# Optimization experiments

Hardware: AMD Instinct MI355X
Metric: run time of the kernel (lower is better)

The kernel has to match this reference:

```python
import jax, jax.numpy as jnp
import numpy as np
import math

N_HEADS = 16
D_KV = 64
D_MODEL = 1024
NUM_BUCKETS = 32
MAX_DISTANCE = 128


def _relative_position_bucket(rel_pos):
    # encoder (is_decoder=False): bidirectional buckets
    num_buckets = NUM_BUCKETS // 2  # 16
    rel_buckets = (rel_pos > 0).astype(jnp.int32) * num_buckets
    rel_pos = jnp.abs(rel_pos)
    max_exact = num_buckets // 2  # 8
    is_small = rel_pos < max_exact
    rel_pos_large = max_exact + (
        jnp.log(rel_pos.astype(jnp.float32) / max_exact)
        / math.log(MAX_DISTANCE / max_exact)
        * (num_buckets - max_exact)
    ).astype(jnp.int32)
    rel_pos_large = jnp.minimum(rel_pos_large, num_buckets - 1)
    return rel_buckets + jnp.where(is_small, rel_pos, rel_pos_large)


def setup_inputs() -> dict:
    key = jax.random.key(0)
    ks = jax.random.split(key, 6)
    s = 1.0 / math.sqrt(D_MODEL)
    return {
        "hidden_states": jax.random.normal(ks[0], (2, 2048, D_MODEL), jnp.float32),
        "Wq": jax.random.normal(ks[1], (D_MODEL, N_HEADS * D_KV), jnp.float32) * s,
        "Wk": jax.random.normal(ks[2], (D_MODEL, N_HEADS * D_KV), jnp.float32) * s,
        "Wv": jax.random.normal(ks[3], (D_MODEL, N_HEADS * D_KV), jnp.float32) * s,
        "Wo": jax.random.normal(ks[4], (N_HEADS * D_KV, D_MODEL), jnp.float32) * s,
        "rel_bias": jax.random.normal(ks[5], (NUM_BUCKETS, N_HEADS), jnp.float32),
    }


def reference(hidden_states, Wq, Wk, Wv, Wo, rel_bias):
    b, seq, _ = hidden_states.shape
    q = (hidden_states @ Wq).reshape(b, seq, N_HEADS, D_KV)
    k = (hidden_states @ Wk).reshape(b, seq, N_HEADS, D_KV)
    v = (hidden_states @ Wv).reshape(b, seq, N_HEADS, D_KV)

    # relative position bias: [1, n_heads, q_len, k_len]
    ctx = jnp.arange(seq, dtype=jnp.int32)[:, None]
    mem = jnp.arange(seq, dtype=jnp.int32)[None, :]
    buckets = _relative_position_bucket(mem - ctx)  # [q, k]
    pos_bias = rel_bias[buckets]                    # [q, k, h]
    pos_bias = jnp.transpose(pos_bias, (2, 0, 1))[None]  # [1, h, q, k]

    # NOTE: T5-style attention has no 1/sqrt(d) scaling
    attn = jnp.einsum('binc,bjnc->bnij', q, k) + pos_bias
    attn = jax.nn.softmax(attn.astype(jnp.float32), axis=-1).astype(attn.dtype)
    o = jnp.einsum('bnij,bjnc->binc', attn, v).reshape(b, seq, N_HEADS * D_KV)
    return o @ Wo
```

## Files before the change

### kernel.cpp

```cpp
#include <hip/hip_runtime.h>
#include <hip/hip_bf16.h>
#include <math.h>

#define DM   1024
#define HD   1024
#define NH   16
#define DK   64
#define SEQ  2048
#define BATCH 2

#define LOG2E 1.4426950408889634f

typedef __attribute__((ext_vector_type(8))) short bf16x8;
typedef __attribute__((ext_vector_type(4))) float f32x4;

static __device__ __forceinline__ short f2b(float f) {
  union { float f; unsigned u; } v; v.f = f;
  unsigned r = (v.u + 0x7fffu + ((v.u >> 16) & 1u)) >> 16;
  return (short)r;
}

static __device__ __forceinline__ void gload_lds16(const void* g, void* l) {
  __builtin_amdgcn_global_load_lds(
      (const __attribute__((address_space(1))) void*)g,
      (__attribute__((address_space(3))) void*)l, 16, 0, 0);
}


__global__ __launch_bounds__(256) void k_cvt_h(const float* __restrict__ in,
                                               short* __restrict__ out) {
  int i = (blockIdx.x * 256 + threadIdx.x) * 8;
  float4 a = *reinterpret_cast<const float4*>(in + i);
  float4 b = *reinterpret_cast<const float4*>(in + i + 4);
  bf16x8 o;
  o[0] = f2b(a.x); o[1] = f2b(a.y); o[2] = f2b(a.z); o[3] = f2b(a.w);
  o[4] = f2b(b.x); o[5] = f2b(b.y); o[6] = f2b(b.z); o[7] = f2b(b.w);
  *reinterpret_cast<bf16x8*>(out + i) = o;
}

__global__ __launch_bounds__(256) void k_wtrans(const float* __restrict__ Wq,
                                                const float* __restrict__ Wk,
                                                const float* __restrict__ Wv,
                                                const float* __restrict__ Wo,
                                                short* __restrict__ Wts) {
  const float* src = (blockIdx.z == 0) ? Wq : (blockIdx.z == 1) ? Wk
                   : (blockIdx.z == 2) ? Wv : Wo;
  const float scl = (blockIdx.z == 0) ? LOG2E : 1.0f;
  short* dst = Wts + (size_t)blockIdx.z * DM * HD;
  __shared__ float t[32][33];
  int tx = threadIdx.x & 31, ty = threadIdx.x >> 5;
  int k0 = blockIdx.y * 32, n0 = blockIdx.x * 32;
#pragma unroll
  for (int i = 0; i < 4; ++i)
    t[ty + i * 8][tx] = src[(size_t)(k0 + ty + i * 8) * 1024 + n0 + tx];
  __syncthreads();
#pragma unroll
  for (int i = 0; i < 4; ++i)
    dst[(size_t)(n0 + ty + i * 8) * 1024 + k0 + tx] = f2b(t[tx][ty + i * 8] * scl);
}

__global__ __launch_bounds__(256) void k_bias(const float* __restrict__ rel_bias,
                                              float* __restrict__ btab) {
  int idx = blockIdx.x * 256 + threadIdx.x;
  int h = idx >> 12, pos = idx & 4095;
  int delta = pos - 2047;
  int rb = (delta > 0) ? 16 : 0;
  int ar = (delta < 0) ? -delta : delta;
  int bb;
  if (ar < 8) bb = ar;
  else {
    bb = 8 + (int)(logf((float)ar * 0.125f) * (8.0f / 2.7725887222397811f));
    if (bb > 15) bb = 15;
  }
  btab[idx] = rel_bias[(rb + bb) * NH + h] * LOG2E;
}

__global__ __launch_bounds__(256) void k_vtrans(const short* __restrict__ Vb,
                                                short* __restrict__ Vt) {
  int bh = blockIdx.y, b = bh >> 4, h = bh & 15;
  int st = blockIdx.x * 64;
  __shared__ short t[64][72];
  int tx = threadIdx.x & 15, ty = threadIdx.x >> 4;
#pragma unroll
  for (int i = 0; i < 4; ++i) {
    int row = ty + i * 16;
    *reinterpret_cast<short4*>(&t[row][tx * 4]) =
        *reinterpret_cast<const short4*>(
            &Vb[(size_t)(b * SEQ + st + row) * HD + h * 64 + tx * 4]);
  }
  __syncthreads();
  const int chunk = tx >> 3, bb = tx & 7;
  const int p = ((bb & 3) << 1) | (bb >> 2);
  const int kvpos = st + chunk * 32 + p * 4;
#pragma unroll
  for (int i = 0; i < 4; ++i) {
    int dk = ty + i * 16;
    short4 v = make_short4(t[tx * 4 + 0][dk], t[tx * 4 + 1][dk],
                           t[tx * 4 + 2][dk], t[tx * 4 + 3][dk]);
    *reinterpret_cast<short4*>(
        &Vt[(size_t)bh * DK * SEQ + (size_t)dk * SEQ + kvpos]) = v;
  }
}

template <int OUTF32>
__global__ __launch_bounds__(256) void k_gemm_bt(const short* __restrict__ A,
                                                 const short* __restrict__ Bt,
                                                 void* __restrict__ Cv,
                                                 size_t btz, size_t cz) {
  __shared__ __align__(16) short As[128 * 32];
  __shared__ __align__(16) short Bs[128 * 32];
  const int tid = threadIdx.x, w = tid >> 6, lane = tid & 63;
  const int wr = w >> 1, wc = w & 1, lg = lane >> 4, l15 = lane & 15;
  const int rowBase = blockIdx.y * 128, colBase = blockIdx.x * 128;
  const short* B = Bt + (size_t)blockIdx.z * btz;

  f32x4 acc[4][4];
#pragma unroll
  for (int m = 0; m < 4; ++m)
#pragma unroll
    for (int n = 0; n < 4; ++n) acc[m][n] = (f32x4){0.f, 0.f, 0.f, 0.f};

  const int c1 = w * 64 + lane, c2 = c1 + 256;
  const short* Ap1 = A + (size_t)(rowBase + (c1 >> 2)) * 1024 + (c1 & 3) * 8;
  const short* Ap2 = A + (size_t)(rowBase + (c2 >> 2)) * 1024 + (c2 & 3) * 8;
  const short* Bp1 = B + (size_t)(colBase + (c1 >> 2)) * 1024 + (c1 & 3) * 8;
  const short* Bp2 = B + (size_t)(colBase + (c2 >> 2)) * 1024 + (c2 & 3) * 8;
  char* AsB = (char*)As;
  char* BsB = (char*)Bs;

  for (int k0 = 0; k0 < 1024; k0 += 32) {
    __syncthreads();
    gload_lds16(Ap1 + k0, AsB + w * 1024);
    gload_lds16(Ap2 + k0, AsB + 4096 + w * 1024);
    gload_lds16(Bp1 + k0, BsB + w * 1024);
    gload_lds16(Bp2 + k0, BsB + 4096 + w * 1024);
    asm volatile("s_waitcnt vmcnt(0)" ::: "memory");
    __syncthreads();
    bf16x8 af[4], bfr[4];
#pragma unroll
    for (int m = 0; m < 4; ++m)
      af[m] = *reinterpret_cast<const bf16x8*>(
          &As[(wr * 64 + m * 16 + l15) * 32 + lg * 8]);
#pragma unroll
    for (int n = 0; n < 4; ++n)
      bfr[n] = *reinterpret_cast<const bf16x8*>(
          &Bs[(wc * 64 + n * 16 + l15) * 32 + lg * 8]);
#pragma unroll
    for (int m = 0; m < 4; ++m)
#pragma unroll
      for (int n = 0; n < 4; ++n)
        acc[m][n] =
            __builtin_amdgcn_mfma_f32_16x16x32_bf16(af[m], bfr[n], acc[m][n], 0, 0, 0);
  }

#pragma unroll
  for (int m = 0; m < 4; ++m)
#pragma unroll
    for (int n = 0; n < 4; ++n) {
      int col = colBase + wc * 64 + n * 16 + l15;
#pragma unroll
      for (int r = 0; r < 4; ++r) {
        int row = rowBase + wr * 64 + m * 16 + lg * 4 + r;
        if (OUTF32)
          ((float*)Cv)[(size_t)row * 1024 + col] = acc[m][n][r];
        else
          ((short*)Cv + (size_t)blockIdx.z * cz)[(size_t)row * 1024 + col] =
              f2b(acc[m][n][r]);
      }
    }
}

static __device__ __forceinline__ void stage_tile(const char* gbase, size_t grs,
                                                  char* lbase, int w, int lane) {
  const int r0 = w * 16 + (lane >> 3);
  const int cb = (lane & 7) * 16;
  const int sw = (r0 & 7) << 4;
  gload_lds16(gbase + (size_t)r0 * grs + (cb ^ sw), lbase + w * 2048);
  gload_lds16(gbase + (size_t)(r0 + 8) * grs + (cb ^ sw), lbase + w * 2048 + 1024);
}

__global__ __launch_bounds__(256, 4) void k_attn(const short* __restrict__ Qb,
                                                 const short* __restrict__ Kb,
                                                 const short* __restrict__ Vt,
                                                 const float* __restrict__ biasTab,
                                                 short* __restrict__ Ob) {
  const int j = blockIdx.x;
  const int orig = (j & 7) * 128 + (j >> 3);
  const int qt = orig & 31, bh = orig >> 5;
  const int b = bh >> 4, h = bh & 15;
  const int w = threadIdx.x >> 6, lane = threadIdx.x & 63;
  const int lg = lane >> 4, l15 = lane & 15;
  const int qbase = qt * 64 + w * 16;

  __shared__ __align__(16) char Ks[2][8192];
  __shared__ __align__(16) char Vs[2][8192];
  const int swz = (l15 & 7) << 4;

  const short* Qrow = Qb + (size_t)(b * SEQ + qbase + l15) * HD + h * 64 + lg * 8;
  bf16x8 q0 = *reinterpret_cast<const bf16x8*>(Qrow);
  bf16x8 q1 = *reinterpret_cast<const bf16x8*>(Qrow + 32);

  const char* Kg = (const char*)(Kb + (size_t)(b * SEQ) * HD + h * 64);
  const char* Vg = (const char*)(Vt + (size_t)bh * DK * SEQ);
  const float* btab = biasTab + h * 4096 + 2047;
  const float bias_hi = btab[1024];
  const float bias_lo = btab[-1024];

  f32x4 o[4];
#pragma unroll
  for (int c = 0; c < 4; ++c) o[c] = (f32x4){0.f, 0.f, 0.f, 0.f};
  float m_r = -INFINITY, l_r = 0.f;

  const f32x4 z4 = (f32x4){0.f, 0.f, 0.f, 0.f};

  stage_tile(Kg, 2048, Ks[0], w, lane);
  stage_tile(Vg, 4096, Vs[0], w, lane);
  asm volatile("s_waitcnt vmcnt(0)" ::: "memory");
  __syncthreads();
  int cur = 0;

  for (int kt = 0; kt < 32; ++kt) {
    const int kvb = kt * 64;
    const int dkv = kvb - qbase;
    if (kt < 31) {
      stage_tile(Kg + (size_t)(kvb + 64) * 2048, 2048, Ks[cur ^ 1], w, lane);
      stage_tile(Vg + (size_t)(kvb + 64) * 2, 4096, Vs[cur ^ 1], w, lane);
    }
    const char* KsC = Ks[cur];
    f32x4 s[4];
#pragma unroll
    for (int c = 0; c < 4; ++c) {
      const char* kr = KsC + (c * 16 + l15) * 128;
      bf16x8 kf0 = *reinterpret_cast<const bf16x8*>(kr + ((lg * 16) ^ swz));
      bf16x8 kf1 = *reinterpret_cast<const bf16x8*>(kr + ((64 + lg * 16) ^ swz));
      s[c] = __builtin_amdgcn_mfma_f32_16x16x32_bf16(kf0, q0, z4, 0, 0, 0);
      s[c] = __builtin_amdgcn_mfma_f32_16x16x32_bf16(kf1, q1, s[c], 0, 0, 0);
    }
    if (dkv >= 112) {
#pragma unroll
      for (int c = 0; c < 4; ++c)
#pragma unroll
        for (int r = 0; r < 4; ++r) s[c][r] += bias_hi;
    } else if (dkv <= -160) {
#pragma unroll
      for (int c = 0; c < 4; ++c)
#pragma unroll
        for (int r = 0; r < 4; ++r) s[c][r] += bias_lo;
    } else {
#pragma unroll
      for (int c = 0; c < 4; ++c)
#pragma unroll
        for (int r = 0; r < 4; ++r)
          s[c][r] += btab[dkv + c * 16 + lg * 4 + r - l15];
    }
    float t0 = fmaxf(fmaxf(s[0][0], s[0][1]), fmaxf(s[0][2], s[0][3]));
    float t1 = fmaxf(fmaxf(s[1][0], s[1][1]), fmaxf(s[1][2], s[1][3]));
    float t2 = fmaxf(fmaxf(s[2][0], s[2][1]), fmaxf(s[2][2], s[2][3]));
    float t3 = fmaxf(fmaxf(s[3][0], s[3][1]), fmaxf(s[3][2], s[3][3]));
    float mx = fmaxf(fmaxf(t0, t1), fmaxf(t2, t3));
    mx = fmaxf(mx, __shfl_xor(mx, 16, 64));
    mx = fmaxf(mx, __shfl_xor(mx, 32, 64));
    if (!__all(mx <= m_r + 8.0f)) {
      float mn = fmaxf(m_r, mx);
      float sc = __builtin_exp2f(m_r - mn);
      m_r = mn;
      l_r *= sc;
#pragma unroll
      for (int c = 0; c < 4; ++c)
#pragma unroll
        for (int r = 0; r < 4; ++r) o[c][r] *= sc;
    }
#pragma unroll
    for (int c = 0; c < 4; ++c)
#pragma unroll
      for (int r = 0; r < 4; ++r) s[c][r] = __builtin_exp2f(s[c][r] - m_r);
    float r0 = (s[0][0] + s[0][1]) + (s[0][2] + s[0][3]);
    float r1 = (s[1][0] + s[1][1]) + (s[1][2] + s[1][3]);
    float r2 = (s[2][0] + s[2][1]) + (s[2][2] + s[2][3]);
    float r3 = (s[3][0] + s[3][1]) + (s[3][2] + s[3][3]);
    float rs = (r0 + r1) + (r2 + r3);
    rs += __shfl_xor(rs, 16, 64);
    rs += __shfl_xor(rs, 32, 64);
    l_r += rs;
    bf16x8 pb0, pb1;
#pragma unroll
    for (int r = 0; r < 4; ++r) {
      pb0[r]     = f2b(s[0][r]);
      pb0[4 + r] = f2b(s[1][r]);
      pb1[r]     = f2b(s[2][r]);
      pb1[4 + r] = f2b(s[3][r]);
    }
    const char* VsC = Vs[cur];
#pragma unroll
    for (int d = 0; d < 4; ++d) {
      const char* vr = VsC + (d * 16 + l15) * 128;
      bf16x8 v0 = *reinterpret_cast<const bf16x8*>(vr + ((lg * 16) ^ swz));
      bf16x8 v1 = *reinterpret_cast<const bf16x8*>(vr + ((64 + lg * 16) ^ swz));
      o[d] = __builtin_amdgcn_mfma_f32_16x16x32_bf16(v0, pb0, o[d], 0, 0, 0);
      o[d] = __builtin_amdgcn_mfma_f32_16x16x32_bf16(v1, pb1, o[d], 0, 0, 0);
    }
    asm volatile("s_waitcnt vmcnt(0)" ::: "memory");
    __syncthreads();
    cur ^= 1;
  }
  float inv = 1.0f / l_r;
  const size_t orow = (size_t)(b * SEQ + qbase + l15) * HD + h * 64;
#pragma unroll
  for (int d = 0; d < 4; ++d) {
    short4 pk;
    pk.x = f2b(o[d][0] * inv); pk.y = f2b(o[d][1] * inv);
    pk.z = f2b(o[d][2] * inv); pk.w = f2b(o[d][3] * inv);
    *reinterpret_cast<short4*>(&Ob[orow + d * 16 + lg * 4]) = pk;
  }
}

extern "C" void kernel_launch(void* const* d_in, const int* in_sizes, int n_in,
                              void* d_out, int out_size, void* d_ws, size_t ws_size,
                              hipStream_t stream) {
  const float* H    = (const float*)d_in[0];
  const float* Wq   = (const float*)d_in[1];
  const float* Wk   = (const float*)d_in[2];
  const float* Wv   = (const float*)d_in[3];
  const float* Wo   = (const float*)d_in[4];
  const float* relb = (const float*)d_in[5];

  char* ws = (char*)d_ws;
  short* Hb   = (short*)(ws);
  short* Wts  = (short*)(ws + ((size_t)8 << 20));
  short* Qb   = (short*)(ws + ((size_t)16 << 20));
  short* Kb   = (short*)(ws + ((size_t)24 << 20));
  short* Vb   = (short*)(ws + ((size_t)32 << 20));
  short* Vt   = (short*)(ws + ((size_t)40 << 20));
  short* Ob   = (short*)(ws + ((size_t)48 << 20));
  float* btab = (float*)(ws + ((size_t)56 << 20));

  k_cvt_h<<<2048, 256, 0, stream>>>(H, Hb);
  k_wtrans<<<dim3(32, 32, 4), 256, 0, stream>>>(Wq, Wk, Wv, Wo, Wts);
  k_bias<<<256, 256, 0, stream>>>(relb, btab);

  k_gemm_bt<0><<<dim3(8, 32, 3), 256, 0, stream>>>(
      Hb, Wts, Qb, (size_t)1024 * 1024, (size_t)4096 * 1024);

  k_vtrans<<<dim3(32, 32), 256, 0, stream>>>(Vb, Vt);
  k_attn<<<1024, 256, 0, stream>>>(Qb, Kb, Vt, btab, Ob);

  k_gemm_bt<1><<<dim3(8, 32, 1), 256, 0, stream>>>(
      Ob, Wts + (size_t)3 * 1024 * 1024, d_out, 0, 0);
}
```

Before: 234.2 us.

## Use packed bf16 convert, fold uniform bias into max, add MFMA priority hints

Replaces the software round-to-nearest bf16 conversion with the hardware v_cvt_pk_bf16_f32 instruction in the attention inner loop and the epilogue. For tiles where the relative-position bias is uniform, the bias is no longer added to all 16 scores; it is added once to the row max and subtracted from the exp2 offset instead. The max reduction is rebalanced into three-input fmax chains, and s_setprio is raised around the MFMA sections so waves issuing matrix ops get scheduling priority. The aim is fewer VALU instructions per tile in the softmax path. The hardware convert may round slightly differently from the software routine.

```diff
diff --git a/kernel.cpp b/kernel.cpp
--- a/kernel.cpp
+++ b/kernel.cpp
@@ -18,6 +18,12 @@
   union { float f; unsigned u; } v; v.f = f;
   unsigned r = (v.u + 0x7fffu + ((v.u >> 16) & 1u)) >> 16;
   return (short)r;
+}
+
+static __device__ __forceinline__ int cvt_pk(float lo, float hi) {
+  int r;
+  asm("v_cvt_pk_bf16_f32 %0, %1, %2" : "=v"(r) : "v"(lo), "v"(hi));
+  return r;
 }
 
 static __device__ __forceinline__ void gload_lds16(const void* g, void* l) {
@@ -228,6 +234,7 @@
     }
     const char* KsC = Ks[cur];
     f32x4 s[4];
+    __builtin_amdgcn_s_setprio(1);
 #pragma unroll
     for (int c = 0; c < 4; ++c) {
       const char* kr = KsC + (c * 16 + l15) * 128;
@@ -236,16 +243,12 @@
       s[c] = __builtin_amdgcn_mfma_f32_16x16x32_bf16(kf0, q0, z4, 0, 0, 0);
       s[c] = __builtin_amdgcn_mfma_f32_16x16x32_bf16(kf1, q1, s[c], 0, 0, 0);
     }
+    __builtin_amdgcn_s_setprio(0);
+    float bu = 0.f;
     if (dkv >= 112) {
-#pragma unroll
-      for (int c = 0; c < 4; ++c)
-#pragma unroll
-        for (int r = 0; r < 4; ++r) s[c][r] += bias_hi;
+      bu = bias_hi;
     } else if (dkv <= -160) {
-#pragma unroll
-      for (int c = 0; c < 4; ++c)
-#pragma unroll
-        for (int r = 0; r < 4; ++r) s[c][r] += bias_lo;
+      bu = bias_lo;
     } else {
 #pragma unroll
       for (int c = 0; c < 4; ++c)
@@ -253,13 +256,17 @@
         for (int r = 0; r < 4; ++r)
           s[c][r] += btab[dkv + c * 16 + lg * 4 + r - l15];
     }
-    float t0 = fmaxf(fmaxf(s[0][0], s[0][1]), fmaxf(s[0][2], s[0][3]));
-    float t1 = fmaxf(fmaxf(s[1][0], s[1][1]), fmaxf(s[1][2], s[1][3]));
-    float t2 = fmaxf(fmaxf(s[2][0], s[2][1]), fmaxf(s[2][2], s[2][3]));
-    float t3 = fmaxf(fmaxf(s[3][0], s[3][1]), fmaxf(s[3][2], s[3][3]));
-    float mx = fmaxf(fmaxf(t0, t1), fmaxf(t2, t3));
+    float u0 = fmaxf(fmaxf(s[0][0], s[0][1]), s[0][2]);
+    float u1 = fmaxf(fmaxf(s[0][3], s[1][0]), s[1][1]);
+    float u2 = fmaxf(fmaxf(s[1][2], s[1][3]), s[2][0]);
+    float u3 = fmaxf(fmaxf(s[2][1], s[2][2]), s[2][3]);
+    float u4 = fmaxf(fmaxf(s[3][0], s[3][1]), s[3][2]);
+    float v0 = fmaxf(fmaxf(u0, u1), u2);
+    float v1 = fmaxf(fmaxf(u3, u4), s[3][3]);
+    float mx = fmaxf(v0, v1);
     mx = fmaxf(mx, __shfl_xor(mx, 16, 64));
     mx = fmaxf(mx, __shfl_xor(mx, 32, 64));
+    mx += bu;
     if (!__all(mx <= m_r + 8.0f)) {
       float mn = fmaxf(m_r, mx);
       float sc = __builtin_exp2f(m_r - mn);
@@ -270,10 +277,11 @@
 #pragma unroll
         for (int r = 0; r < 4; ++r) o[c][r] *= sc;
     }
+    const float mb = m_r - bu;
 #pragma unroll
     for (int c = 0; c < 4; ++c)
 #pragma unroll
-      for (int r = 0; r < 4; ++r) s[c][r] = __builtin_exp2f(s[c][r] - m_r);
+      for (int r = 0; r < 4; ++r) s[c][r] = __builtin_exp2f(s[c][r] - mb);
     float r0 = (s[0][0] + s[0][1]) + (s[0][2] + s[0][3]);
     float r1 = (s[1][0] + s[1][1]) + (s[1][2] + s[1][3]);
     float r2 = (s[2][0] + s[2][1]) + (s[2][2] + s[2][3]);
@@ -282,23 +290,24 @@
     rs += __shfl_xor(rs, 16, 64);
     rs += __shfl_xor(rs, 32, 64);
     l_r += rs;
-    bf16x8 pb0, pb1;
-#pragma unroll
-    for (int r = 0; r < 4; ++r) {
-      pb0[r]     = f2b(s[0][r]);
-      pb0[4 + r] = f2b(s[1][r]);
-      pb1[r]     = f2b(s[2][r]);
-      pb1[4 + r] = f2b(s[3][r]);
-    }
+    int4 p0i, p1i;
+    p0i.x = cvt_pk(s[0][0], s[0][1]); p0i.y = cvt_pk(s[0][2], s[0][3]);
+    p0i.z = cvt_pk(s[1][0], s[1][1]); p0i.w = cvt_pk(s[1][2], s[1][3]);
+    p1i.x = cvt_pk(s[2][0], s[2][1]); p1i.y = cvt_pk(s[2][2], s[2][3]);
+    p1i.z = cvt_pk(s[3][0], s[3][1]); p1i.w = cvt_pk(s[3][2], s[3][3]);
+    bf16x8 pb0 = *reinterpret_cast<bf16x8*>(&p0i);
+    bf16x8 pb1 = *reinterpret_cast<bf16x8*>(&p1i);
     const char* VsC = Vs[cur];
+    __builtin_amdgcn_s_setprio(1);
 #pragma unroll
     for (int d = 0; d < 4; ++d) {
       const char* vr = VsC + (d * 16 + l15) * 128;
-      bf16x8 v0 = *reinterpret_cast<const bf16x8*>(vr + ((lg * 16) ^ swz));
-      bf16x8 v1 = *reinterpret_cast<const bf16x8*>(vr + ((64 + lg * 16) ^ swz));
-      o[d] = __builtin_amdgcn_mfma_f32_16x16x32_bf16(v0, pb0, o[d], 0, 0, 0);
-      o[d] = __builtin_amdgcn_mfma_f32_16x16x32_bf16(v1, pb1, o[d], 0, 0, 0);
-    }
+      bf16x8 v0f = *reinterpret_cast<const bf16x8*>(vr + ((lg * 16) ^ swz));
+      bf16x8 v1f = *reinterpret_cast<const bf16x8*>(vr + ((64 + lg * 16) ^ swz));
+      o[d] = __builtin_amdgcn_mfma_f32_16x16x32_bf16(v0f, pb0, o[d], 0, 0, 0);
+      o[d] = __builtin_amdgcn_mfma_f32_16x16x32_bf16(v1f, pb1, o[d], 0, 0, 0);
+    }
+    __builtin_amdgcn_s_setprio(0);
     asm volatile("s_waitcnt vmcnt(0)" ::: "memory");
     __syncthreads();
     cur ^= 1;
@@ -307,10 +316,10 @@
   const size_t orow = (size_t)(b * SEQ + qbase + l15) * HD + h * 64;
 #pragma unroll
   for (int d = 0; d < 4; ++d) {
-    short4 pk;
-    pk.x = f2b(o[d][0] * inv); pk.y = f2b(o[d][1] * inv);
-    pk.z = f2b(o[d][2] * inv); pk.w = f2b(o[d][3] * inv);
-    *reinterpret_cast<short4*>(&Ob[orow + d * 16 + lg * 4]) = pk;
+    int2 e;
+    e.x = cvt_pk(o[d][0] * inv, o[d][1] * inv);
+    e.y = cvt_pk(o[d][2] * inv, o[d][3] * inv);
+    *reinterpret_cast<int2*>(&Ob[orow + d * 16 + lg * 4]) = e;
   }
 }
 
```

Result: faster. 221.0 us (-5.6%).
